# Kernel tuning notes

Hardware: AMD Instinct MI355X
Metric: run time of the kernel (lower is better)

Reference implementation:

```python
import jax, jax.numpy as jnp
import numpy as np

NEG_SLOPE = 0.2  # PyG GATConv default negative_slope


def gat_conv(x, src, dst, W, a_src, a_dst, b, N):
    """Single PyG-style GATConv (add_self_loops already applied via src/dst).
    x: [N, F_in], W: [F_in, H*C], a_src/a_dst: [H, C], b: [H*C].
    Returns [N, H*C] (concat=True)."""
    H, C = a_src.shape
    h = (x @ W).reshape(N, H, C)                      # [N,H,C]
    alpha_src = jnp.sum(h * a_src[None], axis=-1)      # [N,H]
    alpha_dst = jnp.sum(h * a_dst[None], axis=-1)      # [N,H]
    e = jax.nn.leaky_relu(alpha_src[src] + alpha_dst[dst], NEG_SLOPE)  # [E,H]
    # numerically stable segment softmax over incoming edges of each dst node
    m = jax.ops.segment_max(e, dst, num_segments=N)    # [N,H]
    m = jnp.where(jnp.isfinite(m), m, 0.0)
    ex = jnp.exp(e - m[dst])                           # [E,H]
    den = jax.ops.segment_sum(ex, dst, num_segments=N) # [N,H]
    alpha = ex / (den[dst] + 1e-16)                    # [E,H]
    out = jax.ops.segment_sum(h[src] * alpha[..., None], dst, num_segments=N)  # [N,H,C]
    return out.reshape(N, H * C) + b


def setup_inputs() -> dict:
    key = jax.random.key(0)
    ks = jax.random.split(key, 9)
    B, N, E = 2, 50000, 800000
    d_model, n_hidden, en_dim, H = 128, 128, 64, 1
    fea_mats = jax.random.normal(ks[0], (B, N, d_model), dtype=jnp.float32)
    edge_index = jax.random.randint(ks[1], (B, 2, E), 0, N, dtype=jnp.int32)
    s1 = 1.0 / np.sqrt(d_model)
    s2 = 1.0 / np.sqrt(n_hidden)
    return {
        "fea_mats": fea_mats,
        "edge_index": edge_index,
        "W1": jax.random.normal(ks[2], (d_model, H * n_hidden), dtype=jnp.float32) * s1,
        "att_src1": jax.random.normal(ks[3], (H, n_hidden), dtype=jnp.float32) * s2,
        "att_dst1": jax.random.normal(ks[4], (H, n_hidden), dtype=jnp.float32) * s2,
        "b1": jnp.zeros((H * n_hidden,), dtype=jnp.float32),
        "W2": jax.random.normal(ks[5], (H * n_hidden, H * en_dim), dtype=jnp.float32) * s2,
        "att_src2": jax.random.normal(ks[6], (H, en_dim), dtype=jnp.float32) / np.sqrt(en_dim),
        "att_dst2": jax.random.normal(ks[7], (H, en_dim), dtype=jnp.float32) / np.sqrt(en_dim),
        "b2": jnp.zeros((H * en_dim,), dtype=jnp.float32),
    }


def reference(fea_mats, edge_index, W1, att_src1, att_dst1, b1, W2, att_src2, att_dst2, b2):
    B, N, _ = fea_mats.shape
    loops = jnp.arange(N, dtype=edge_index.dtype)

    def per_graph(x, ei):
        # PyG GATConv adds self-loops by default
        src = jnp.concatenate([ei[0], loops])
        dst = jnp.concatenate([ei[1], loops])
        h = gat_conv(x, src, dst, W1, att_src1, att_dst1, b1, N)
        h = jax.nn.relu(h)
        h = gat_conv(h, src, dst, W2, att_src2, att_dst2, b2, N)
        return h  # [N, en_dim]

    return jax.vmap(per_graph)(fea_mats, edge_index)  # [B, N, en_dim]
```

## Files before the change

kernel.cpp:

```cpp
#include <hip/hip_runtime.h>

#define NEG_SLOPE 0.2f
static constexpr int BLK = 256;
static constexpr int EPB = 4096;
static constexpr int CAP = 6144;

typedef short bf16x8 __attribute__((ext_vector_type(8)));
typedef float f32x4  __attribute__((ext_vector_type(4)));
typedef unsigned short u16x8 __attribute__((ext_vector_type(8)));
typedef unsigned short u16x4 __attribute__((ext_vector_type(4)));

template<int NE> struct uvec_t;
template<> struct uvec_t<4>{ using T = u16x4; };
template<> struct uvec_t<8>{ using T = u16x8; };

static inline int cdiv(long a, long b){ return (int)((a + b - 1) / b); }

__device__ __forceinline__ unsigned short f2bf(float f){
    unsigned u = __float_as_uint(f);
    u += 0x7fff + ((u >> 16) & 1);
    return (unsigned short)(u >> 16);
}
__device__ __forceinline__ float bf2f(unsigned short h){
    return __uint_as_float(((unsigned)h) << 16);
}

struct GP {
    const int* src; const int* dst; const float* X;
    int* gcnt; int* gbase; int* ebuf; int* rowptr; int* csrsrc;
    unsigned short* h1b; float* agg1; unsigned short* h2b;
    float *as1, *ad1, *as2, *ad2; float* outp;
};

template<int CO, int CT, bool RELU_IN, bool BF16OUT>
__device__ __forceinline__ void gemm_dev(
    int bid, const float* __restrict__ X,
    const unsigned short* __restrict__ Wt_hi, const unsigned short* __restrict__ Wt_lo,
    const float* __restrict__ avs, const float* __restrict__ avd,
    void* __restrict__ Hout, float* __restrict__ as_out, float* __restrict__ ad_out,
    int N, unsigned short* smem)
{
    constexpr int CHUNKS = CO / (CT * 16);
    constexpr int HWB = CT * 4096;
    int ch, rtb;
    if (CHUNKS == 1){ ch = 0; rtb = bid; } else { ch = bid & 1; rtb = bid >> 1; }
    int c0 = ch * (CT * 16);

    {
        const char* srch = (const char*)(Wt_hi + (size_t)c0 * 128);
        const char* srcl = (const char*)(Wt_lo + (size_t)c0 * 128);
        #pragma unroll
        for (int it = 0; it < CT * 2; ++it){
            int o = (it * 256 + (int)threadIdx.x) * 16;
            const char* sp = (o < HWB) ? (srch + o) : (srcl + (o - HWB));
            u16x8 v = *(const u16x8*)sp;
            int so = o ^ (((o >> 8) & 7) << 4);
            *(u16x8*)((char*)smem + so) = v;
        }
    }
    __syncthreads();

    int wave = threadIdx.x >> 6;
    int lane = threadIdx.x & 63;
    int rt = rtb * 4 + wave;
    if (rt >= (N >> 4)) return;
    int r0 = rt << 4;
    int rl = lane & 15, g = lane >> 4;
    const float* xrow = X + (long)(r0 + rl) * 128 + g * 8;

    f32x4 acc[CT];
    #pragma unroll
    for (int t = 0; t < CT; t++) acc[t] = (f32x4)(0.f);

    int sw = (rl & 7) << 4;
    #pragma unroll
    for (int ks = 0; ks < 4; ks++){
        float4 xa = *(const float4*)(xrow + ks * 32);
        float4 xb = *(const float4*)(xrow + ks * 32 + 4);
        float xv[8] = {xa.x, xa.y, xa.z, xa.w, xb.x, xb.y, xb.z, xb.w};
        bf16x8 xbf;
        #pragma unroll
        for (int j = 0; j < 8; j++){
            float x = xv[j];
            if (RELU_IN) x = fmaxf(x, 0.f);
            xbf[j] = (short)f2bf(x);
        }
        int rbase = rl * 256 + ks * 64 + g * 16;
        #pragma unroll
        for (int t = 0; t < CT; t++){
            bf16x8 wh = *(const bf16x8*)((char*)smem + ((t * 4096 + rbase) ^ sw));
            bf16x8 wl = *(const bf16x8*)((char*)smem + ((HWB + t * 4096 + rbase) ^ sw));
            acc[t] = __builtin_amdgcn_mfma_f32_16x16x32_bf16(wh, xbf, acc[t], 0, 0, 0);
            acc[t] = __builtin_amdgcn_mfma_f32_16x16x32_bf16(wl, xbf, acc[t], 0, 0, 0);
        }
    }

    float ps = 0.f, pd = 0.f;
    #pragma unroll
    for (int t = 0; t < CT; t++){
        int c = c0 + t * 16 + 4 * g;
        float4 vs4 = *(const float4*)(avs + c);
        float4 vd4 = *(const float4*)(avd + c);
        ps += acc[t][0]*vs4.x + acc[t][1]*vs4.y + acc[t][2]*vs4.z + acc[t][3]*vs4.w;
        pd += acc[t][0]*vd4.x + acc[t][1]*vd4.y + acc[t][2]*vd4.z + acc[t][3]*vd4.w;
        long base = (long)(r0 + rl) * CO + c;
        if (BF16OUT){
            u16x4 pk;
            #pragma unroll
            for (int r = 0; r < 4; r++) pk[r] = f2bf(acc[t][r]);
            *(u16x4*)((unsigned short*)Hout + base) = pk;
        } else {
            float4 pv;
            pv.x = acc[t][0]; pv.y = acc[t][1]; pv.z = acc[t][2]; pv.w = acc[t][3];
            *(float4*)((float*)Hout + base) = pv;
        }
    }
    ps += __shfl_xor(ps, 16, 64); ps += __shfl_xor(ps, 32, 64);
    pd += __shfl_xor(pd, 16, 64); pd += __shfl_xor(pd, 32, 64);
    if (g == 0){
        unsafeAtomicAdd(as_out + r0 + rl, ps);
        unsafeAtomicAdd(ad_out + r0 + rl, pd);
    }
}

__device__ __forceinline__ void bucket_dev(
    int bid, const GP* __restrict__ g, int E, int Etot, int nbk, unsigned short* smem)
{
    int* spk   = (int*)smem;
    int* shist = spk + 4096;
    int* sbase = shist + 256;
    int tid = (int)threadIdx.x;
    for (int i = tid; i < nbk; i += 256) shist[i] = 0;
    __syncthreads();
    int e0 = bid * EPB;
    #pragma unroll
    for (int i = 0; i < EPB / 256; i++){
        int idx = i * 256 + tid; int e = e0 + idx;
        unsigned p = 0xFFFFFFFFu;
        if (e < Etot){
            int s, d;
            if (e < E){ s = g->src[e]; d = g->dst[e]; } else { s = e - E; d = s; }
            p = ((unsigned)s << 16) | (unsigned)d;
            atomicAdd(&shist[d >> 8], 1);
        }
        spk[idx] = (int)p;
    }
    __syncthreads();
    for (int i = tid; i < nbk; i += 256){
        sbase[i] = atomicAdd(&g->gcnt[i], shist[i]);
        shist[i] = 0;
    }
    __syncthreads();
    #pragma unroll
    for (int i = 0; i < EPB / 256; i++){
        int idx = i * 256 + tid;
        unsigned p = (unsigned)spk[idx];
        if (p != 0xFFFFFFFFu){
            int d = (int)(p & 0xFFFFu); int b = d >> 8;
            int r = sbase[b] + atomicAdd(&shist[b], 1);
            if (r < CAP) g->ebuf[(size_t)b * CAP + r] = (int)p;
        }
    }
}

__device__ __forceinline__ void fine_dev(int k, const GP* __restrict__ g, int N, int Etot)
{
    __shared__ int pk2[CAP];
    __shared__ int fs[256];
    __shared__ int fill[256];
    __shared__ int fh[256];
    int tid = (int)threadIdx.x;
    int cnt = min(g->gcnt[k], CAP);
    int bb  = g->gbase[k];
    for (int i = tid; i < cnt; i += 256) pk2[i] = g->ebuf[(size_t)k * CAP + i];
    fh[tid] = 0; fill[tid] = 0;
    __syncthreads();
    for (int i = tid; i < cnt; i += 256) atomicAdd(&fh[pk2[i] & 255], 1);
    __syncthreads();
    int v = fh[tid];
    fs[tid] = v;
    __syncthreads();
    #pragma unroll
    for (int off = 1; off < 256; off <<= 1){
        int t = (tid >= off) ? fs[tid - off] : 0;
        __syncthreads();
        fs[tid] += t;
        __syncthreads();
    }
    int excl = fs[tid] - v;
    __syncthreads();
    fs[tid] = excl;
    __syncthreads();
    int node = k * 256 + tid;
    if (node < N) g->rowptr[node] = bb + excl;
    if (k == 0 && tid == 0) g->rowptr[N] = Etot;
    for (int i = tid; i < cnt; i += 256){
        unsigned p = (unsigned)pk2[i];
        int f = (int)(p & 255u);
        int r = atomicAdd(&fill[f], 1);
        g->csrsrc[bb + fs[f] + r] = (int)(p >> 16);
    }
}

template<int CO, bool BF16H>
__device__ __forceinline__ void agg_dev(
    int bid, const int* __restrict__ rowptr, const int* __restrict__ csr_src,
    const float* __restrict__ as, const float* __restrict__ ad,
    const void* __restrict__ h, const float* __restrict__ bias,
    float* __restrict__ out, int N)
{
    constexpr int ELEMS = CO / 16;
    using uvec = typename uvec_t<ELEMS>::T;
    int node = bid * (BLK / 64) + (threadIdx.x >> 6);
    int lane = threadIdx.x & 63;
    if (node >= N) return;
    int start = rowptr[node];
    int deg   = rowptr[node + 1] - start;
    float adv = ad[node];
    int g  = lane >> 4;
    int ql = lane & 15;

    const unsigned short* hb = (const unsigned short*)h;
    const float*          hf = (const float*)h;

    if (deg <= 64){
        int   s = 0;
        float e = -1e30f;
        if (lane < deg){
            s = csr_src[start + lane];
            float v = as[s] + adv;
            e = v > 0.f ? v : NEG_SLOPE * v;
        }
        float m = e;
        #pragma unroll
        for (int off = 32; off; off >>= 1) m = fmaxf(m, __shfl_xor(m, off, 64));
        float ex = (lane < deg) ? __expf(e - m) : 0.f;
        float sum = ex;
        #pragma unroll
        for (int off = 32; off; off >>= 1) sum += __shfl_xor(sum, off, 64);
        float alpha = ex / (sum + 1e-16f);

        float acc[ELEMS];
        #pragma unroll
        for (int i = 0; i < ELEMS; i++) acc[i] = 0.f;

        int j = 0;
        for (; j + 7 < deg; j += 8){
            int e0 = j + g, e1 = j + 4 + g;
            int   s0 = __shfl(s, e0, 64),      s1 = __shfl(s, e1, 64);
            float a0 = __shfl(alpha, e0, 64),  a1 = __shfl(alpha, e1, 64);
            if (BF16H){
                uvec h0 = *(const uvec*)(hb + (long)s0 * CO + ql * ELEMS);
                uvec h1 = *(const uvec*)(hb + (long)s1 * CO + ql * ELEMS);
                #pragma unroll
                for (int i = 0; i < ELEMS; i++)
                    acc[i] += a0 * bf2f(h0[i]) + a1 * bf2f(h1[i]);
            } else {
                float4 h0 = *(const float4*)(hf + (long)s0 * CO + ql * ELEMS);
                float4 h1 = *(const float4*)(hf + (long)s1 * CO + ql * ELEMS);
                acc[0]       += a0 * h0.x + a1 * h1.x;
                acc[1]       += a0 * h0.y + a1 * h1.y;
                acc[2]       += a0 * h0.z + a1 * h1.z;
                acc[ELEMS-1] += a0 * h0.w + a1 * h1.w;
            }
        }
        for (; j + 3 < deg; j += 4){
            int e0 = j + g;
            int   s0 = __shfl(s, e0, 64);
            float a0 = __shfl(alpha, e0, 64);
            if (BF16H){
                uvec h0 = *(const uvec*)(hb + (long)s0 * CO + ql * ELEMS);
                #pragma unroll
                for (int i = 0; i < ELEMS; i++) acc[i] += a0 * bf2f(h0[i]);
            } else {
                float4 h0 = *(const float4*)(hf + (long)s0 * CO + ql * ELEMS);
                acc[0] += a0 * h0.x; acc[1] += a0 * h0.y;
                acc[2] += a0 * h0.z; acc[ELEMS-1] += a0 * h0.w;
            }
        }
        if (j < deg){
            int rem = deg - j;
            int e0 = min(j + g, deg - 1);
            int   s0 = __shfl(s, e0, 64);
            float a0 = __shfl(alpha, e0, 64);
            if (g < rem){
                if (BF16H){
                    uvec h0 = *(const uvec*)(hb + (long)s0 * CO + ql * ELEMS);
                    #pragma unroll
                    for (int i = 0; i < ELEMS; i++) acc[i] += a0 * bf2f(h0[i]);
                } else {
                    float4 h0 = *(const float4*)(hf + (long)s0 * CO + ql * ELEMS);
                    acc[0] += a0 * h0.x; acc[1] += a0 * h0.y;
                    acc[2] += a0 * h0.z; acc[ELEMS-1] += a0 * h0.w;
                }
            }
        }
        #pragma unroll
        for (int i = 0; i < ELEMS; i++){
            acc[i] += __shfl_xor(acc[i], 16, 64);
            acc[i] += __shfl_xor(acc[i], 32, 64);
        }
        if (g == 0){
            float* o = out + (long)node * CO + ql * ELEMS;
            #pragma unroll
            for (int i = 0; i < ELEMS; i += 4){
                float4 ov;
                ov.x = acc[i+0] + bias[ql * ELEMS + i + 0];
                ov.y = acc[i+1] + bias[ql * ELEMS + i + 1];
                ov.z = acc[i+2] + bias[ql * ELEMS + i + 2];
                ov.w = acc[i+3] + bias[ql * ELEMS + i + 3];
                *(float4*)(o + i) = ov;
            }
        }
    } else {
        constexpr int VPL = CO / 64;
        float accf[VPL];
        #pragma unroll
        for (int i = 0; i < VPL; i++) accf[i] = 0.f;
        float m = -1e30f;
        for (int jj = lane; jj < deg; jj += 64){
            int sj = csr_src[start + jj];
            float v = as[sj] + adv; v = v > 0.f ? v : NEG_SLOPE * v;
            m = fmaxf(m, v);
        }
        #pragma unroll
        for (int off = 32; off; off >>= 1) m = fmaxf(m, __shfl_xor(m, off, 64));
        float sum = 0.f;
        for (int jj = lane; jj < deg; jj += 64){
            int sj = csr_src[start + jj];
            float v = as[sj] + adv; v = v > 0.f ? v : NEG_SLOPE * v;
            sum += __expf(v - m);
        }
        #pragma unroll
        for (int off = 32; off; off >>= 1) sum += __shfl_xor(sum, off, 64);
        float inv = 1.f / (sum + 1e-16f);
        for (int jj = 0; jj < deg; jj++){
            int sj = csr_src[start + jj];
            float v = as[sj] + adv; v = v > 0.f ? v : NEG_SLOPE * v;
            float aj = __expf(v - m) * inv;
            if (BF16H){
                const unsigned short* hr = hb + (long)sj * CO + lane * VPL;
                #pragma unroll
                for (int i = 0; i < VPL; i++) accf[i] += aj * bf2f(hr[i]);
            } else {
                const float* hr = hf + (long)sj * CO + lane * VPL;
                #pragma unroll
                for (int i = 0; i < VPL; i++) accf[i] += aj * hr[i];
            }
        }
        float* o = out + (long)node * CO + lane * VPL;
        #pragma unroll
        for (int i = 0; i < VPL; i++) o[i] = accf[i] + bias[lane * VPL + i];
    }
}

__global__ __launch_bounds__(BLK) void prep_k(
    const float* __restrict__ W1, const float* __restrict__ W2,
    unsigned short* __restrict__ w1h, unsigned short* __restrict__ w1l,
    unsigned short* __restrict__ w2h, unsigned short* __restrict__ w2l)
{
    int i = blockIdx.x * BLK + threadIdx.x;
    if (i < 128 * 128){
        int c = i >> 7, k = i & 127;
        float w = W1[k * 128 + c];
        unsigned short hi = f2bf(w);
        w1h[i] = hi; w1l[i] = f2bf(w - bf2f(hi));
        if (i < 64 * 128){
            float w2 = W2[k * 64 + c];
            unsigned short hi2 = f2bf(w2);
            w2h[i] = hi2; w2l[i] = f2bf(w2 - bf2f(hi2));
        }
    }
}

__global__ __launch_bounds__(256, 4) void kA(
    GP a, GP b, const unsigned short* __restrict__ w1h, const unsigned short* __restrict__ w1l,
    const float* __restrict__ avs1, const float* __restrict__ avd1,
    int EB_a, int EB_b, int GB_a, int GB_b, int E, int Etot, int N, int nbk)
{
    __shared__ unsigned short smem[16384];
    int bid = blockIdx.x;
    if (bid < EB_a){ bucket_dev(bid, &a, E, Etot, nbk, smem); return; }
    bid -= EB_a;
    if (bid < EB_b){ bucket_dev(bid, &b, E, Etot, nbk, smem); return; }
    bid -= EB_b;
    if (bid < GB_a){ gemm_dev<128,4,false,true>(bid, a.X, w1h, w1l, avs1, avd1, a.h1b, a.as1, a.ad1, N, smem); return; }
    bid -= GB_a;
    if (bid < GB_b) gemm_dev<128,4,false,true>(bid, b.X, w1h, w1l, avs1, avd1, b.h1b, b.as1, b.ad1, N, smem);
}

__global__ __launch_bounds__(256) void kscan(GP a, GP b, int nbk){
    const GP* g = (blockIdx.x == 0) ? &a : &b;
    __shared__ int sh[256];
    int tid = (int)threadIdx.x;
    int v = (tid < nbk) ? g->gcnt[tid] : 0;
    sh[tid] = v;
    __syncthreads();
    #pragma unroll
    for (int off = 1; off < 256; off <<= 1){
        int t = (tid >= off) ? sh[tid - off] : 0;
        __syncthreads();
        sh[tid] += t;
        __syncthreads();
    }
    if (tid < nbk) g->gbase[tid] = sh[tid] - v;
}

__global__ __launch_bounds__(256) void kB(GP a, GP b, int nb_a, int nb_b, int N, int Etot){
    int bid = blockIdx.x; const GP* g; int k;
    if (bid < nb_a){ g = &a; k = bid; }
    else { k = bid - nb_a; if (k >= nb_b) return; g = &b; }
    fine_dev(k, g, N, Etot);
}

__global__ __launch_bounds__(256, 4) void gemm2_k(
    GP a, GP b, const unsigned short* __restrict__ w2h, const unsigned short* __restrict__ w2l,
    const float* __restrict__ avs2, const float* __restrict__ avd2, int GB_a, int GB_b, int N)
{
    __shared__ unsigned short smem[8192];
    int bid = blockIdx.x;
    if (bid < GB_a) gemm_dev<64,2,true,true>(bid, a.agg1, w2h, w2l, avs2, avd2, a.h2b, a.as2, a.ad2, N, smem);
    else { bid -= GB_a; if (bid < GB_b) gemm_dev<64,2,true,true>(bid, b.agg1, w2h, w2l, avs2, avd2, b.h2b, b.as2, b.ad2, N, smem); }
}

template<int CO, bool BF16H>
__global__ __launch_bounds__(BLK) void agg2_k(GP a, GP b, const float* bias, int AB_a, int AB_b, int N){
    int bid = blockIdx.x; const GP* g; int lb;
    if (bid < AB_a){ g = &a; lb = bid; }
    else { lb = bid - AB_a; if (lb >= AB_b) return; g = &b; }
    const float* as; const float* ad; const void* h; float* outp;
    if constexpr (CO == 128){ as = g->as1; ad = g->ad1; h = g->h1b; outp = g->agg1; }
    else                    { as = g->as2; ad = g->ad2; h = g->h2b; outp = g->outp; }
    agg_dev<CO, BF16H>(lb, g->rowptr, g->csrsrc, as, ad, h, bias, outp, N);
}

extern "C" void kernel_launch(void* const* d_in, const int* in_sizes, int n_in,
                              void* d_out, int out_size, void* d_ws, size_t ws_size,
                              hipStream_t stream)
{
    const float* fea  = (const float*)d_in[0];
    const int*   ei   = (const int*)  d_in[1];
    const float* W1   = (const float*)d_in[2];
    const float* av_s1= (const float*)d_in[3];
    const float* av_d1= (const float*)d_in[4];
    const float* b1   = (const float*)d_in[5];
    const float* W2   = (const float*)d_in[6];
    const float* av_s2= (const float*)d_in[7];
    const float* av_d2= (const float*)d_in[8];
    const float* b2   = (const float*)d_in[9];
    float* out = (float*)d_out;

    const int B = 2;
    const int N = out_size / (B * 64);
    const int E = in_sizes[1] / (2 * B);
    const int Etot = E + N;
    const int nbk = (N + 255) >> 8;

    size_t pg = 256 + (size_t)nbk * CAP + (size_t)(N + 2) + (size_t)Etot
              + (size_t)N * (64 + 128 + 32);
    size_t wtf = 8192 + 8192 + 4096 + 4096;
    auto total_f = [&](int ng){ return wtf + (size_t)ng * (4 * (size_t)N + 256) + (size_t)ng * pg + 64; };
    bool fused = (ws_size >= total_f(2) * sizeof(float));
    int NG = fused ? 2 : 1;

    float* ws = (float*)d_ws;
    size_t off = 0;
    unsigned short* w1h = (unsigned short*)(ws + off); off += 8192;
    unsigned short* w1l = (unsigned short*)(ws + off); off += 8192;
    unsigned short* w2h = (unsigned short*)(ws + off); off += 4096;
    unsigned short* w2l = (unsigned short*)(ws + off); off += 4096;

    float* zbase = ws + off;
    size_t znum = (size_t)NG * (4 * (size_t)N + 256);
    off += znum;

    GP g[2];
    for (int gi = 0; gi < NG; gi++){
        GP p;
        p.as1  = zbase + (size_t)gi * (4 * (size_t)N + 256);
        p.ad1  = p.as1 + N;
        p.as2  = p.ad1 + N;
        p.ad2  = p.as2 + N;
        p.gcnt = (int*)(p.ad2 + N);
        p.gbase  = (int*)(ws + off); off += 256;
        p.ebuf   = (int*)(ws + off); off += (size_t)nbk * CAP;
        p.rowptr = (int*)(ws + off); off += (size_t)(N + 2);
        p.csrsrc = (int*)(ws + off); off += Etot;
        p.h1b  = (unsigned short*)(ws + off); off += (size_t)N * 64;
        p.agg1 = ws + off; off += (size_t)N * 128;
        p.h2b  = (unsigned short*)(ws + off); off += (size_t)N * 32;
        g[gi] = p;
    }

    const int RT  = N >> 4;
    const int GB1 = cdiv(RT, 4) * 2;
    const int GB2 = cdiv(RT, 4) * 2;
    const int EBk = cdiv(Etot, EPB);
    const int AB  = cdiv(N, BLK / 64);

    if (fused){
        for (int bi = 0; bi < 2; bi++){
            g[bi].src = ei + (size_t)bi * 2 * E;
            g[bi].dst = g[bi].src + E;
            g[bi].X   = fea + (size_t)bi * N * 128;
            g[bi].outp= out + (size_t)bi * N * 64;
        }
        hipMemsetAsync(zbase, 0, znum * sizeof(float), stream);
        prep_k<<<cdiv(128*128, BLK), BLK, 0, stream>>>(W1, W2, w1h, w1l, w2h, w2l);
        kA<<<2*EBk + 2*GB1, 256, 0, stream>>>(g[0], g[1], w1h, w1l, av_s1, av_d1,
                                              EBk, EBk, GB1, GB1, E, Etot, N, nbk);
        kscan<<<2, 256, 0, stream>>>(g[0], g[1], nbk);
        kB<<<2*nbk, 256, 0, stream>>>(g[0], g[1], nbk, nbk, N, Etot);
        agg2_k<128,true> <<<2*AB, BLK, 0, stream>>>(g[0], g[1], b1, AB, AB, N);
        gemm2_k <<<2*GB2, 256, 0, stream>>>(g[0], g[1], w2h, w2l, av_s2, av_d2, GB2, GB2, N);
        agg2_k<64,true> <<<2*AB, BLK, 0, stream>>>(g[0], g[1], b2, AB, AB, N);
    } else {
        prep_k<<<cdiv(128*128, BLK), BLK, 0, stream>>>(W1, W2, w1h, w1l, w2h, w2l);
        for (int bi = 0; bi < B; bi++){
            GP p = g[0];
            p.src = ei + (size_t)bi * 2 * E;
            p.dst = p.src + E;
            p.X   = fea + (size_t)bi * N * 128;
            p.outp= out + (size_t)bi * N * 64;
            hipMemsetAsync(zbase, 0, znum * sizeof(float), stream);
            kA<<<EBk + GB1, 256, 0, stream>>>(p, p, w1h, w1l, av_s1, av_d1,
                                              EBk, 0, GB1, 0, E, Etot, N, nbk);
            kscan<<<1, 256, 0, stream>>>(p, p, nbk);
            kB<<<nbk, 256, 0, stream>>>(p, p, nbk, 0, N, Etot);
            agg2_k<128,true> <<<AB, BLK, 0, stream>>>(p, p, b1, AB, 0, N);
            gemm2_k <<<GB2, 256, 0, stream>>>(p, p, w2h, w2l, av_s2, av_d2, GB2, 0, N);
            agg2_k<64,true> <<<AB, BLK, 0, stream>>>(p, p, b2, AB, 0, N);
        }
    }
}
```

Before: 230.7 us.

## Assign one 16-lane group per destination node in GAT aggregation

Aggregation now processes four destination nodes per wavefront, one 16-lane group each, instead of one node per 64-lane wavefront. Average degree is about 17, so most lanes previously sat idle during the softmax and gather. Each group computes the segment softmax with 16-wide shuffles and gathers four neighbour rows per iteration to keep more loads in flight. The risks are divergence between groups with different degrees and more register pressure from the unrolled gathers.

```diff
diff --git a/kernel.cpp b/kernel.cpp
--- a/kernel.cpp
+++ b/kernel.cpp
@@ -23,6 +23,9 @@
 }
 __device__ __forceinline__ float bf2f(unsigned short h){
     return __uint_as_float(((unsigned)h) << 16);
+}
+__device__ __forceinline__ float lrelu(float v){
+    return v > 0.f ? v : NEG_SLOPE * v;
 }
 
 struct GP {
@@ -202,155 +205,115 @@
     }
 }
 
-template<int CO, bool BF16H>
+template<int CO>
 __device__ __forceinline__ void agg_dev(
     int bid, const int* __restrict__ rowptr, const int* __restrict__ csr_src,
     const float* __restrict__ as, const float* __restrict__ ad,
-    const void* __restrict__ h, const float* __restrict__ bias,
+    const unsigned short* __restrict__ hb, const float* __restrict__ bias,
     float* __restrict__ out, int N)
 {
     constexpr int ELEMS = CO / 16;
     using uvec = typename uvec_t<ELEMS>::T;
-    int node = bid * (BLK / 64) + (threadIdx.x >> 6);
     int lane = threadIdx.x & 63;
+    int wv   = threadIdx.x >> 6;
+    int grp  = lane >> 4;
+    int ql   = lane & 15;
+    int node = bid * 16 + wv * 4 + grp;
     if (node >= N) return;
     int start = rowptr[node];
     int deg   = rowptr[node + 1] - start;
     float adv = ad[node];
-    int g  = lane >> 4;
-    int ql = lane & 15;
-
-    const unsigned short* hb = (const unsigned short*)h;
-    const float*          hf = (const float*)h;
-
-    if (deg <= 64){
-        int   s = 0;
-        float e = -1e30f;
-        if (lane < deg){
-            s = csr_src[start + lane];
-            float v = as[s] + adv;
-            e = v > 0.f ? v : NEG_SLOPE * v;
-        }
-        float m = e;
-        #pragma unroll
-        for (int off = 32; off; off >>= 1) m = fmaxf(m, __shfl_xor(m, off, 64));
-        float ex = (lane < deg) ? __expf(e - m) : 0.f;
-        float sum = ex;
-        #pragma unroll
-        for (int off = 32; off; off >>= 1) sum += __shfl_xor(sum, off, 64);
-        float alpha = ex / (sum + 1e-16f);
-
-        float acc[ELEMS];
-        #pragma unroll
-        for (int i = 0; i < ELEMS; i++) acc[i] = 0.f;
-
-        int j = 0;
-        for (; j + 7 < deg; j += 8){
-            int e0 = j + g, e1 = j + 4 + g;
-            int   s0 = __shfl(s, e0, 64),      s1 = __shfl(s, e1, 64);
-            float a0 = __shfl(alpha, e0, 64),  a1 = __shfl(alpha, e1, 64);
-            if (BF16H){
-                uvec h0 = *(const uvec*)(hb + (long)s0 * CO + ql * ELEMS);
-                uvec h1 = *(const uvec*)(hb + (long)s1 * CO + ql * ELEMS);
-                #pragma unroll
-                for (int i = 0; i < ELEMS; i++)
-                    acc[i] += a0 * bf2f(h0[i]) + a1 * bf2f(h1[i]);
-            } else {
-                float4 h0 = *(const float4*)(hf + (long)s0 * CO + ql * ELEMS);
-                float4 h1 = *(const float4*)(hf + (long)s1 * CO + ql * ELEMS);
-                acc[0]       += a0 * h0.x + a1 * h1.x;
-                acc[1]       += a0 * h0.y + a1 * h1.y;
-                acc[2]       += a0 * h0.z + a1 * h1.z;
-                acc[ELEMS-1] += a0 * h0.w + a1 * h1.w;
-            }
-        }
-        for (; j + 3 < deg; j += 4){
-            int e0 = j + g;
-            int   s0 = __shfl(s, e0, 64);
-            float a0 = __shfl(alpha, e0, 64);
-            if (BF16H){
-                uvec h0 = *(const uvec*)(hb + (long)s0 * CO + ql * ELEMS);
-                #pragma unroll
-                for (int i = 0; i < ELEMS; i++) acc[i] += a0 * bf2f(h0[i]);
-            } else {
-                float4 h0 = *(const float4*)(hf + (long)s0 * CO + ql * ELEMS);
-                acc[0] += a0 * h0.x; acc[1] += a0 * h0.y;
-                acc[2] += a0 * h0.z; acc[ELEMS-1] += a0 * h0.w;
-            }
-        }
-        if (j < deg){
-            int rem = deg - j;
-            int e0 = min(j + g, deg - 1);
-            int   s0 = __shfl(s, e0, 64);
-            float a0 = __shfl(alpha, e0, 64);
-            if (g < rem){
-                if (BF16H){
-                    uvec h0 = *(const uvec*)(hb + (long)s0 * CO + ql * ELEMS);
-                    #pragma unroll
-                    for (int i = 0; i < ELEMS; i++) acc[i] += a0 * bf2f(h0[i]);
-                } else {
-                    float4 h0 = *(const float4*)(hf + (long)s0 * CO + ql * ELEMS);
-                    acc[0] += a0 * h0.x; acc[1] += a0 * h0.y;
-                    acc[2] += a0 * h0.z; acc[ELEMS-1] += a0 * h0.w;
-                }
-            }
-        }
-        #pragma unroll
-        for (int i = 0; i < ELEMS; i++){
-            acc[i] += __shfl_xor(acc[i], 16, 64);
-            acc[i] += __shfl_xor(acc[i], 32, 64);
-        }
-        if (g == 0){
-            float* o = out + (long)node * CO + ql * ELEMS;
+
+    int   sv0 = 0, sv1 = 0, sv2 = 0, sv3 = 0;
+    float ev0 = -1e30f, ev1 = -1e30f, ev2 = -1e30f, ev3 = -1e30f;
+    if (ql < deg)      { sv0 = csr_src[start + ql];      ev0 = lrelu(as[sv0] + adv); }
+    if (16 + ql < deg) { sv1 = csr_src[start + 16 + ql]; ev1 = lrelu(as[sv1] + adv); }
+    if (32 + ql < deg) { sv2 = csr_src[start + 32 + ql]; ev2 = lrelu(as[sv2] + adv); }
+    if (48 + ql < deg) { sv3 = csr_src[start + 48 + ql]; ev3 = lrelu(as[sv3] + adv); }
+
+    float m = fmaxf(fmaxf(ev0, ev1), fmaxf(ev2, ev3));
+    if (deg > 64){
+        for (int j = 64 + ql; j < deg; j += 16){
+            int sj = csr_src[start + j];
+            m = fmaxf(m, lrelu(as[sj] + adv));
+        }
+    }
+    #pragma unroll
+    for (int off = 8; off; off >>= 1) m = fmaxf(m, __shfl_xor(m, off, 16));
+
+    float x0 = (ql < deg)      ? __expf(ev0 - m) : 0.f;
+    float x1 = (16 + ql < deg) ? __expf(ev1 - m) : 0.f;
+    float x2 = (32 + ql < deg) ? __expf(ev2 - m) : 0.f;
+    float x3 = (48 + ql < deg) ? __expf(ev3 - m) : 0.f;
+    float sum = x0 + x1 + x2 + x3;
+    if (deg > 64){
+        for (int j = 64 + ql; j < deg; j += 16){
+            int sj = csr_src[start + j];
+            sum += __expf(lrelu(as[sj] + adv) - m);
+        }
+    }
+    #pragma unroll
+    for (int off = 8; off; off >>= 1) sum += __shfl_xor(sum, off, 16);
+    float inv = 1.f / (sum + 1e-16f);
+    float a0 = x0 * inv, a1 = x1 * inv, a2 = x2 * inv, a3 = x3 * inv;
+
+    float acc[ELEMS];
+    #pragma unroll
+    for (int i = 0; i < ELEMS; i++) acc[i] = 0.f;
+
+    #pragma unroll
+    for (int q = 0; q < 4; q++){
+        int rem = deg - q * 16;
+        if (rem <= 0) break;
+        int lim = rem < 16 ? rem : 16;
+        float aq; int sq;
+        if      (q == 0){ aq = a0; sq = sv0; }
+        else if (q == 1){ aq = a1; sq = sv1; }
+        else if (q == 2){ aq = a2; sq = sv2; }
+        else            { aq = a3; sq = sv3; }
+        int t = 0;
+        for (; t + 3 < lim; t += 4){
+            int   sA = __shfl(sq, t, 16),   sB = __shfl(sq, t+1, 16);
+            int   sC = __shfl(sq, t+2, 16), sD = __shfl(sq, t+3, 16);
+            float aA = __shfl(aq, t, 16),   aB = __shfl(aq, t+1, 16);
+            float aC = __shfl(aq, t+2, 16), aD = __shfl(aq, t+3, 16);
+            uvec rA = *(const uvec*)(hb + (long)sA * CO + ql * ELEMS);
+            uvec rB = *(const uvec*)(hb + (long)sB * CO + ql * ELEMS);
+            uvec rC = *(const uvec*)(hb + (long)sC * CO + ql * ELEMS);
+            uvec rD = *(const uvec*)(hb + (long)sD * CO + ql * ELEMS);
             #pragma unroll
-            for (int i = 0; i < ELEMS; i += 4){
-                float4 ov;
-                ov.x = acc[i+0] + bias[ql * ELEMS + i + 0];
-                ov.y = acc[i+1] + bias[ql * ELEMS + i + 1];
-                ov.z = acc[i+2] + bias[ql * ELEMS + i + 2];
-                ov.w = acc[i+3] + bias[ql * ELEMS + i + 3];
-                *(float4*)(o + i) = ov;
-            }
-        }
-    } else {
-        constexpr int VPL = CO / 64;
-        float accf[VPL];
-        #pragma unroll
-        for (int i = 0; i < VPL; i++) accf[i] = 0.f;
-        float m = -1e30f;
-        for (int jj = lane; jj < deg; jj += 64){
-            int sj = csr_src[start + jj];
-            float v = as[sj] + adv; v = v > 0.f ? v : NEG_SLOPE * v;
-            m = fmaxf(m, v);
-        }
-        #pragma unroll
-        for (int off = 32; off; off >>= 1) m = fmaxf(m, __shfl_xor(m, off, 64));
-        float sum = 0.f;
-        for (int jj = lane; jj < deg; jj += 64){
-            int sj = csr_src[start + jj];
-            float v = as[sj] + adv; v = v > 0.f ? v : NEG_SLOPE * v;
-            sum += __expf(v - m);
-        }
-        #pragma unroll
-        for (int off = 32; off; off >>= 1) sum += __shfl_xor(sum, off, 64);
-        float inv = 1.f / (sum + 1e-16f);
-        for (int jj = 0; jj < deg; jj++){
-            int sj = csr_src[start + jj];
-            float v = as[sj] + adv; v = v > 0.f ? v : NEG_SLOPE * v;
-            float aj = __expf(v - m) * inv;
-            if (BF16H){
-                const unsigned short* hr = hb + (long)sj * CO + lane * VPL;
-                #pragma unroll
-                for (int i = 0; i < VPL; i++) accf[i] += aj * bf2f(hr[i]);
-            } else {
-                const float* hr = hf + (long)sj * CO + lane * VPL;
-                #pragma unroll
-                for (int i = 0; i < VPL; i++) accf[i] += aj * hr[i];
-            }
-        }
-        float* o = out + (long)node * CO + lane * VPL;
-        #pragma unroll
-        for (int i = 0; i < VPL; i++) o[i] = accf[i] + bias[lane * VPL + i];
+            for (int i = 0; i < ELEMS; i++)
+                acc[i] += aA * bf2f(rA[i]) + aB * bf2f(rB[i])
+                        + aC * bf2f(rC[i]) + aD * bf2f(rD[i]);
+        }
+        for (; t < lim; t++){
+            int   sA = __shfl(sq, t, 16);
+            float aA = __shfl(aq, t, 16);
+            uvec rA = *(const uvec*)(hb + (long)sA * CO + ql * ELEMS);
+            #pragma unroll
+            for (int i = 0; i < ELEMS; i++) acc[i] += aA * bf2f(rA[i]);
+        }
+        if (lim < 16) break;
+    }
+    if (deg > 64){
+        for (int j = 64; j < deg; j++){
+            int sj = csr_src[start + j];
+            float aj = __expf(lrelu(as[sj] + adv) - m) * inv;
+            uvec rA = *(const uvec*)(hb + (long)sj * CO + ql * ELEMS);
+            #pragma unroll
+            for (int i = 0; i < ELEMS; i++) acc[i] += aj * bf2f(rA[i]);
+        }
+    }
+
+    float* o = out + (long)node * CO + ql * ELEMS;
+    #pragma unroll
+    for (int i = 0; i < ELEMS; i += 4){
+        float4 ov;
+        ov.x = acc[i+0] + bias[ql * ELEMS + i + 0];
+        ov.y = acc[i+1] + bias[ql * ELEMS + i + 1];
+        ov.z = acc[i+2] + bias[ql * ELEMS + i + 2];
+        ov.w = acc[i+3] + bias[ql * ELEMS + i + 3];
+        *(float4*)(o + i) = ov;
     }
 }
 
@@ -423,15 +386,15 @@
     else { bid -= GB_a; if (bid < GB_b) gemm_dev<64,2,true,true>(bid, b.agg1, w2h, w2l, avs2, avd2, b.h2b, b.as2, b.ad2, N, smem); }
 }
 
-template<int CO, bool BF16H>
+template<int CO>
 __global__ __launch_bounds__(BLK) void agg2_k(GP a, GP b, const float* bias, int AB_a, int AB_b, int N){
     int bid = blockIdx.x; const GP* g; int lb;
     if (bid < AB_a){ g = &a; lb = bid; }
     else { lb = bid - AB_a; if (lb >= AB_b) return; g = &b; }
-    const float* as; const float* ad; const void* h; float* outp;
+    const float* as; const float* ad; const unsigned short* h; float* outp;
     if constexpr (CO == 128){ as = g->as1; ad = g->ad1; h = g->h1b; outp = g->agg1; }
     else                    { as = g->as2; ad = g->ad2; h = g->h2b; outp = g->outp; }
-    agg_dev<CO, BF16H>(lb, g->rowptr, g->csrsrc, as, ad, h, bias, outp, N);
+    agg_dev<CO>(lb, g->rowptr, g->csrsrc, as, ad, h, bias, outp, N);
 }
 
 extern "C" void kernel_launch(void* const* d_in, const int* in_sizes, int n_in,
@@ -496,7 +459,7 @@
     const int GB1 = cdiv(RT, 4) * 2;
     const int GB2 = cdiv(RT, 4) * 2;
     const int EBk = cdiv(Etot, EPB);
-    const int AB  = cdiv(N, BLK / 64);
+    const int AB  = cdiv(N, 16);
 
     if (fused){
         for (int bi = 0; bi < 2; bi++){
@@ -511,9 +474,9 @@
                                               EBk, EBk, GB1, GB1, E, Etot, N, nbk);
         kscan<<<2, 256, 0, stream>>>(g[0], g[1], nbk);
         kB<<<2*nbk, 256, 0, stream>>>(g[0], g[1], nbk, nbk, N, Etot);
-        agg2_k<128,true> <<<2*AB, BLK, 0, stream>>>(g[0], g[1], b1, AB, AB, N);
+        agg2_k<128><<<2*AB, BLK, 0, stream>>>(g[0], g[1], b1, AB, AB, N);
         gemm2_k <<<2*GB2, 256, 0, stream>>>(g[0], g[1], w2h, w2l, av_s2, av_d2, GB2, GB2, N);
-        agg2_k<64,true> <<<2*AB, BLK, 0, stream>>>(g[0], g[1], b2, AB, AB, N);
+        agg2_k<64> <<<2*AB, BLK, 0, stream>>>(g[0], g[1], b2, AB, AB, N);
     } else {
         prep_k<<<cdiv(128*128, BLK), BLK, 0, stream>>>(W1, W2, w1h, w1l, w2h, w2l);
         for (int bi = 0; bi < B; bi++){
@@ -527,9 +490,9 @@
                                               EBk, 0, GB1, 0, E, Etot, N, nbk);
             kscan<<<1, 256, 0, stream>>>(p, p, nbk);
             kB<<<nbk, 256, 0, stream>>>(p, p, nbk, 0, N, Etot);
-            agg2_k<128,true> <<<AB, BLK, 0, stream>>>(p, p, b1, AB, 0, N);
+            agg2_k<128><<<AB, BLK, 0, stream>>>(p, p, b1, AB, 0, N);
             gemm2_k <<<GB2, 256, 0, stream>>>(p, p, w2h, w2l, av_s2, av_d2, GB2, 0, N);
-            agg2_k<64,true> <<<AB, BLK, 0, stream>>>(p, p, b2, AB, 0, N);
-        }
-    }
-}
+            agg2_k<64> <<<AB, BLK, 0, stream>>>(p, p, b2, AB, 0, N);
+        }
+    }
+}
```

Result: faster. 213.7 us (-7.4%).
